# Kernel optimization log

Hardware: AMD Instinct MI355X
Metric: run time of the kernel (lower is better)

The kernel has to match this reference:

```python
import jax, jax.numpy as jnp
import numpy as np

B, L, W, C = 16, 200, 64, 128
H_INTRA = 64   # intra_hidden // 2 per direction
H_INTER = 128
EPS = 1e-8


def layer_norm(x, gamma, beta):
    mu = jnp.mean(x, axis=-1, keepdims=True)
    var = jnp.mean(jnp.square(x - mu), axis=-1, keepdims=True)
    return (x - mu) * jax.lax.rsqrt(var + EPS) * gamma + beta


def gru_seq(x, Wk, Uk, b, H):
    """Keras GRU, reset_after=False, recurrent_activation=sigmoid. x: [N,T,D] -> [N,T,H]."""
    xw = jnp.einsum('ntd,dk->ntk', x, Wk) + b  # precompute input projections [N,T,3H]
    def step(h, xw_t):
        z = jax.nn.sigmoid(xw_t[:, :H] + h @ Uk[:, :H])
        r = jax.nn.sigmoid(xw_t[:, H:2 * H] + h @ Uk[:, H:2 * H])
        hh = jnp.tanh(xw_t[:, 2 * H:] + (r * h) @ Uk[:, 2 * H:])
        h = z * h + (1.0 - z) * hh
        return h, h
    h0 = jnp.zeros((x.shape[0], H), x.dtype)
    _, ys = jax.lax.scan(step, h0, jnp.swapaxes(xw, 0, 1))  # [T,N,H]
    return jnp.swapaxes(ys, 0, 1)


def skip_gru_seq(x, Wk, Uk, b, Wp, bp, H):
    """Skip-RNN GRU (Campos et al.): binary update gate u_t conditionally updates state.
    Returns (outputs [N,T,H], gates [N,T,1])."""
    xw = jnp.einsum('ntd,dk->ntk', x, Wk) + b
    def step(carry, xw_t):
        h, ut = carry
        # straight-through binarization of cumulative update prob
        u = ut + jax.lax.stop_gradient(jnp.round(ut) - ut)  # [N,1]
        z = jax.nn.sigmoid(xw_t[:, :H] + h @ Uk[:, :H])
        r = jax.nn.sigmoid(xw_t[:, H:2 * H] + h @ Uk[:, H:2 * H])
        hh = jnp.tanh(xw_t[:, 2 * H:] + (r * h) @ Uk[:, 2 * H:])
        h_new = z * h + (1.0 - z) * hh
        h = u * h_new + (1.0 - u) * h  # skip: copy state when u == 0
        delta = jax.nn.sigmoid(h @ Wp + bp)  # [N,1]
        ut_next = u * delta + (1.0 - u) * (ut + jnp.minimum(delta, 1.0 - ut))
        return (h, ut_next), (h, u)
    N = x.shape[0]
    h0 = jnp.zeros((N, H), x.dtype)
    ut0 = jnp.ones((N, 1), x.dtype)
    _, (ys, us) = jax.lax.scan(step, (h0, ut0), jnp.swapaxes(xw, 0, 1))
    return jnp.swapaxes(ys, 0, 1), jnp.swapaxes(us, 0, 1)


def setup_inputs():
    key = jax.random.key(0)
    ks = jax.random.split(key, 16)
    rn = lambda k, s: jax.random.normal(k, s, dtype=jnp.float32) * 0.05
    z = lambda s: jnp.zeros(s, jnp.float32)
    o = lambda s: jnp.ones(s, jnp.float32)
    return {
        'x': jax.random.normal(ks[0], (B, L, W, C), dtype=jnp.float32),
        'scale': jax.random.uniform(ks[1], (B, L, W, 1), dtype=jnp.float32),
        'Wf': rn(ks[2], (C, 3 * H_INTRA)), 'Uf': rn(ks[3], (H_INTRA, 3 * H_INTRA)), 'bf': z((3 * H_INTRA,)),
        'Wb': rn(ks[4], (C, 3 * H_INTRA)), 'Ub': rn(ks[5], (H_INTRA, 3 * H_INTRA)), 'bb': z((3 * H_INTRA,)),
        'W_intra_fc': rn(ks[6], (2 * H_INTRA, C)), 'b_intra_fc': z((C,)),
        'g_intra': o((C,)), 'beta_intra': z((C,)),
        'Wi': rn(ks[7], (C + 1, 3 * H_INTER)), 'Ui': rn(ks[8], (H_INTER, 3 * H_INTER)), 'bi': z((3 * H_INTER,)),
        'Wp': rn(ks[9], (H_INTER, 1)), 'bp': z((1,)),
        'W_inter_fc': rn(ks[10], (H_INTER, C)), 'b_inter_fc': z((C,)),
        'g_inter': o((C,)), 'beta_inter': z((C,)),
    }


def reference(x, scale, Wf, Uf, bf, Wb, Ub, bb, W_intra_fc, b_intra_fc, g_intra, beta_intra,
              Wi, Ui, bi, Wp, bp, W_inter_fc, b_inter_fc, g_inter, beta_inter):
    # ----- intra path: bidirectional GRU over the width axis -----
    intra_in = x.reshape(B * L, W, C)
    out_f = gru_seq(intra_in, Wf, Uf, bf, H_INTRA)
    out_b = gru_seq(intra_in[:, ::-1, :], Wb, Ub, bb, H_INTRA)[:, ::-1, :]
    intra_rnn_out = jnp.concatenate([out_f, out_b], axis=-1)  # [B*L, W, 2H]
    update_gate_intra = jnp.ones((64, L), jnp.float32)  # skip=0 branch: constant ones
    intra_dense = intra_rnn_out @ W_intra_fc + b_intra_fc  # [B*L, W, C]
    intra_out = x + layer_norm(intra_dense.reshape(B, L, W, C), g_intra, beta_intra)
    # ----- inter path: skip-GRU over the L (time) axis -----
    inter_in = jnp.transpose(intra_out, (0, 2, 1, 3)).reshape(B * W, L, C)
    scale2 = jnp.transpose(scale, (0, 2, 1, 3)).reshape(B * W, L, 1)
    inter_in = jnp.concatenate([inter_in, scale2], axis=-1)  # [B*W, L, C+1]
    inter_rnn_out, gates = skip_gru_seq(inter_in, Wi, Ui, bi, Wp, bp, H_INTER)
    update_gate_inter = gates[:, :, 0]  # [B*W, L]
    inter_dense = (inter_rnn_out @ W_inter_fc + b_inter_fc).reshape(B, W, L, C)
    inter_ln_in = jnp.transpose(inter_dense, (0, 2, 1, 3))  # [B, L, W, C]
    inter_out = intra_out + layer_norm(inter_ln_in, g_inter, beta_inter)
    return inter_out, update_gate_intra, update_gate_inter
```

## Files before the change

### kernel.cpp

```cpp
#include <hip/hip_runtime.h>
#include <cmath>


__device__ __forceinline__ float sigf(float x) { return 1.0f / (1.0f + expf(-x)); }
__device__ __forceinline__ float rlanef(float v, int l) {
  return __uint_as_float(__builtin_amdgcn_readlane(__float_as_uint(v), (unsigned)l));
}

__global__ __launch_bounds__(256) void k_fill_ones(float* __restrict__ p, int n) {
  int i = blockIdx.x * 256 + threadIdx.x;
  if (i < n) p[i] = 1.0f;
}

enum { MA_X_FWD = 0, MA_X_BWD = 1, MA_INTER = 2 };

template <int MODE>
__global__ __launch_bounds__(256) void k_gemm_xw(
    const float* __restrict__ A0, const float* __restrict__ A1,
    const float* __restrict__ Bm, const float* __restrict__ bias,
    float* __restrict__ Cm, long M0, int N, int K, int KT)
{
  __shared__ float As[16][68];
  __shared__ float Bs[16][68];
  const int tid = threadIdx.x;
  const int tx = tid & 15, ty = tid >> 4;
  const long row0g = M0 + (long)blockIdx.x * 64;
  const int col0 = blockIdx.y * 64;
  const int lr = tid >> 2;
  const int lk4 = (tid & 3) * 4;
  const int bk = tid >> 4;
  const int bc4 = (tid & 15) * 4;
  float acc[4][4];
#pragma unroll
  for (int i = 0; i < 4; ++i)
#pragma unroll
    for (int j = 0; j < 4; ++j) acc[i][j] = 0.f;

  for (int kt = 0; kt < KT; ++kt) {
    const int k0 = kt * 16;
    {
      const long rg = row0g + lr;
      float v0, v1, v2, v3;
      if (MODE == MA_X_FWD) {
        const float4 a4 = *reinterpret_cast<const float4*>(&A0[rg * 128 + k0 + lk4]);
        v0 = a4.x; v1 = a4.y; v2 = a4.z; v3 = a4.w;
      } else if (MODE == MA_X_BWD) {
        const long s = rg >> 6; const int t = (int)(rg & 63);
        const float4 a4 =
            *reinterpret_cast<const float4*>(&A0[(s * 64 + (63 - t)) * 128 + k0 + lk4]);
        v0 = a4.x; v1 = a4.y; v2 = a4.z; v3 = a4.w;
      } else {
        const int n = (int)(rg & 1023);
        const int l = (int)(rg >> 10);
        const long rowc = ((long)(n >> 6) * 200 + l) * 64 + (n & 63);
        const long base = rowc * 128;
        if (kt < 8) {
          const float4 a4 = *reinterpret_cast<const float4*>(&A0[base + k0 + lk4]);
          v0 = a4.x; v1 = a4.y; v2 = a4.z; v3 = a4.w;
        } else {
          v0 = (lk4 == 0) ? A1[rowc] : 0.f;
          v1 = 0.f; v2 = 0.f; v3 = 0.f;
        }
      }
      As[lk4 + 0][lr] = v0;
      As[lk4 + 1][lr] = v1;
      As[lk4 + 2][lr] = v2;
      As[lk4 + 3][lr] = v3;
    }
    {
      const int k = k0 + bk;
      float4 b4 = make_float4(0.f, 0.f, 0.f, 0.f);
      if (k < K) b4 = *reinterpret_cast<const float4*>(&Bm[(long)k * N + col0 + bc4]);
      *reinterpret_cast<float4*>(&Bs[bk][bc4]) = b4;
    }
    __syncthreads();
#pragma unroll
    for (int kk = 0; kk < 16; ++kk) {
      const float4 a4 = *reinterpret_cast<const float4*>(&As[kk][ty * 4]);
      const float4 b4 = *reinterpret_cast<const float4*>(&Bs[kk][tx * 4]);
      const float av[4] = {a4.x, a4.y, a4.z, a4.w};
      const float bv[4] = {b4.x, b4.y, b4.z, b4.w};
#pragma unroll
      for (int i = 0; i < 4; ++i)
#pragma unroll
        for (int j = 0; j < 4; ++j) acc[i][j] = fmaf(av[i], bv[j], acc[i][j]);
    }
    __syncthreads();
  }
  const float4 bi4 = *reinterpret_cast<const float4*>(&bias[col0 + tx * 4]);
  const float bv[4] = {bi4.x, bi4.y, bi4.z, bi4.w};
#pragma unroll
  for (int i = 0; i < 4; ++i) {
    const long rl = (long)blockIdx.x * 64 + ty * 4 + i;
    float4 o;
    o.x = acc[i][0] + bv[0];
    o.y = acc[i][1] + bv[1];
    o.z = acc[i][2] + bv[2];
    o.w = acc[i][3] + bv[3];
    *reinterpret_cast<float4*>(&Cm[rl * (long)N + col0 + tx * 4]) = o;
  }
}

__global__ __launch_bounds__(256, 4) void k_gru_intra2(
    const float* __restrict__ xwf, const float* __restrict__ xwb,
    const float* __restrict__ Uf, const float* __restrict__ Ub,
    float* __restrict__ rnn)
{
  const int dir = blockIdx.y;
  const float* __restrict__ xw = dir ? xwb : xwf;
  const float* __restrict__ U  = dir ? Ub : Uf;
  __shared__ float h8[4][64], z8[4][64], rh8[4][64];
  __shared__ float pA[4][2][128];
  __shared__ float pB[4][2][64];
  const int tid = threadIdx.x;
  const int w = tid >> 6, lane = tid & 63;
  const long s0 = (long)blockIdx.x * 4;
  const bool isZR = (w < 2);
  const int ksZ = w;
  const int ksH = w - 2;

  float ua[32], ub[32];
  if (isZR) {
#pragma unroll
    for (int k = 0; k < 32; ++k) {
      ua[k] = U[(ksZ * 32 + k) * 192 + lane];
      ub[k] = U[(ksZ * 32 + k) * 192 + 64 + lane];
    }
  } else {
#pragma unroll
    for (int k = 0; k < 32; ++k)
      ua[k] = U[(ksH * 32 + k) * 192 + 128 + lane];
  }
  h8[w][lane] = 0.f;
  __syncthreads();

  const long xrow0 = (s0 + w) * 64;
  float xa1 = xw[xrow0 * 192 + lane];
  float xa2 = xw[xrow0 * 192 + 64 + lane];
  float xb  = xw[xrow0 * 192 + 128 + lane];

  for (int t = 0; t < 64; ++t) {
    const int tn = (t < 63) ? t + 1 : t;
    const float xa1n = xw[(xrow0 + tn) * 192 + lane];
    const float xa2n = xw[(xrow0 + tn) * 192 + 64 + lane];
    const float xbn  = xw[(xrow0 + tn) * 192 + 128 + lane];
    if (isZR) {
      const float hv0 = h8[lane >> 5][ksZ * 32 + (lane & 31)];
      const float hv1 = h8[2 + (lane >> 5)][ksZ * 32 + (lane & 31)];
      float az[4], ar[4];
#pragma unroll
      for (int s = 0; s < 4; ++s) { az[s] = 0.f; ar[s] = 0.f; }
#pragma unroll
      for (int s = 0; s < 4; ++s) {
        const float hvr = (s < 2) ? hv0 : hv1;
#pragma unroll
        for (int k = 0; k < 32; ++k) {
          const float hs = rlanef(hvr, ((s & 1) << 5) | k);
          az[s] = fmaf(ua[k], hs, az[s]);
          ar[s] = fmaf(ub[k], hs, ar[s]);
        }
      }
#pragma unroll
      for (int s = 0; s < 4; ++s) {
        pA[s][ksZ][lane] = az[s];
        pA[s][ksZ][64 + lane] = ar[s];
      }
    }
    __syncthreads();
    {
      const float sz = pA[w][0][lane] + pA[w][1][lane] + xa1;
      const float sr = pA[w][0][64 + lane] + pA[w][1][64 + lane] + xa2;
      z8[w][lane] = sigf(sz);
      rh8[w][lane] = sigf(sr) * h8[w][lane];
    }
    __syncthreads();
    if (!isZR) {
      const float rv0 = rh8[lane >> 5][ksH * 32 + (lane & 31)];
      const float rv1 = rh8[2 + (lane >> 5)][ksH * 32 + (lane & 31)];
      float ah[4];
#pragma unroll
      for (int s = 0; s < 4; ++s) ah[s] = 0.f;
#pragma unroll
      for (int s = 0; s < 4; ++s) {
        const float rvr = (s < 2) ? rv0 : rv1;
#pragma unroll
        for (int k = 0; k < 32; ++k) {
          const float rs = rlanef(rvr, ((s & 1) << 5) | k);
          ah[s] = fmaf(ua[k], rs, ah[s]);
        }
      }
#pragma unroll
      for (int s = 0; s < 4; ++s) pB[s][ksH][lane] = ah[s];
    }
    __syncthreads();
    {
      const float pre = pB[w][0][lane] + pB[w][1][lane] + xb;
      const float hh = tanhf(pre);
      const float z = z8[w][lane];
      const float ho = h8[w][lane];
      const float hn = z * ho + (1.f - z) * hh;
      h8[w][lane] = hn;
      const int tt = dir ? (63 - t) : t;
      rnn[((s0 + w) * 64 + tt) * 128 + dir * 64 + lane] = hn;
    }
    __syncthreads();
    xa1 = xa1n; xa2 = xa2n; xb = xbn;
  }
}

__global__ __launch_bounds__(1024, 4) void k_gru_inter3(
    const float* __restrict__ xw, const float* __restrict__ Ui,
    const float* __restrict__ Wp, const float* __restrict__ bp,
    float* __restrict__ rnn, float* __restrict__ gates,
    float* __restrict__ hstate, float* __restrict__ ustate,
    int t0, int nt)
{
  __shared__ float h4[4][128], z4[4][128], rh4[4][128];
  __shared__ float pA[4][8][256];
  __shared__ float pB[4][8][128];
  __shared__ float uu[4], utt[4];
  const int tid = threadIdx.x;
  const int w = tid >> 6, lane = tid & 63;
  const int n0 = blockIdx.x * 4;
  const bool isZR = (w < 8);

  float ureg[64];
  if (isZR) {
#pragma unroll
    for (int j = 0; j < 4; ++j)
#pragma unroll
      for (int k = 0; k < 16; ++k)
        ureg[j * 16 + k] = Ui[(long)(w * 16 + k) * 384 + j * 64 + lane];
  } else {
    const int ks = w - 8;
#pragma unroll
    for (int j = 0; j < 2; ++j)
#pragma unroll
      for (int k = 0; k < 16; ++k)
        ureg[j * 16 + k] = Ui[(long)(ks * 16 + k) * 384 + 256 + j * 64 + lane];
  }
  if (tid < 512) {
    const int s = tid >> 7, c = tid & 127;
    h4[s][c] = (t0 == 0) ? 0.f : hstate[(long)(n0 + s) * 128 + c];
  }
  if (tid < 4) {
    utt[tid] = (t0 == 0) ? 1.f : ustate[n0 + tid];
    uu[tid]  = (t0 == 0) ? 1.f : ustate[1024 + n0 + tid];
  }
  const float bp0 = bp[0];
  float wprA = 0.f, wprB = 0.f;
  if (w < 4) { wprA = Wp[lane]; wprB = Wp[64 + lane]; }
  __syncthreads();

  const int cs = w >> 2;
  const int cc = (w & 3) * 64 + lane;
  float xc = xw[(long)(n0 + cs) * 384 + cc];
  float xbA = 0.f, xbB = 0.f;
  if (w < 4) {
    xbA = xw[(long)(n0 + w) * 384 + 256 + lane];
    xbB = xw[(long)(n0 + w) * 384 + 320 + lane];
  }

  for (int dl = 0; dl < nt; ++dl) {
    const float u0g = uu[0], u1g = uu[1], u2g = uu[2], u3g = uu[3];
    const bool act = (u0g + u1g + u2g + u3g) != 0.f;
    const int dn = (dl + 1 < nt) ? dl + 1 : dl;
    const float xcn = xw[((long)dn * 1024 + n0 + cs) * 384 + cc];
    float xbAn = 0.f, xbBn = 0.f;
    if (w < 4) {
      xbAn = xw[((long)dn * 1024 + n0 + w) * 384 + 256 + lane];
      xbBn = xw[((long)dn * 1024 + n0 + w) * 384 + 320 + lane];
    }
    if (act) {
      if (isZR) {
        const float hv = h4[lane >> 4][w * 16 + (lane & 15)];
        float acc[4][4];
#pragma unroll
        for (int j = 0; j < 4; ++j)
#pragma unroll
          for (int s = 0; s < 4; ++s) acc[j][s] = 0.f;
#pragma unroll
        for (int s = 0; s < 4; ++s) {
          const float ug = (s == 0) ? u0g : (s == 1) ? u1g : (s == 2) ? u2g : u3g;
          if (ug != 0.f) {
#pragma unroll
            for (int k = 0; k < 16; ++k) {
              const float hs = rlanef(hv, (s << 4) | k);
              acc[0][s] = fmaf(ureg[k], hs, acc[0][s]);
              acc[1][s] = fmaf(ureg[16 + k], hs, acc[1][s]);
              acc[2][s] = fmaf(ureg[32 + k], hs, acc[2][s]);
              acc[3][s] = fmaf(ureg[48 + k], hs, acc[3][s]);
            }
#pragma unroll
            for (int j = 0; j < 4; ++j) pA[s][w][j * 64 + lane] = acc[j][s];
          }
        }
      }
      __syncthreads();
      {
        const float ugc = uu[cs];
        if (ugc != 0.f) {
          float sum = xc;
#pragma unroll
          for (int ks = 0; ks < 8; ++ks) sum += pA[cs][ks][cc];
          if (cc < 128) z4[cs][cc] = sigf(sum);
          else rh4[cs][cc - 128] = sigf(sum) * h4[cs][cc - 128];
        }
      }
      __syncthreads();
      if (!isZR) {
        const int ks = w - 8;
        const float rv = rh4[lane >> 4][ks * 16 + (lane & 15)];
        float acc0[4], acc1[4];
#pragma unroll
        for (int s = 0; s < 4; ++s) { acc0[s] = 0.f; acc1[s] = 0.f; }
#pragma unroll
        for (int s = 0; s < 4; ++s) {
          const float ug = (s == 0) ? u0g : (s == 1) ? u1g : (s == 2) ? u2g : u3g;
          if (ug != 0.f) {
#pragma unroll
            for (int k = 0; k < 16; ++k) {
              const float rs = rlanef(rv, (s << 4) | k);
              acc0[s] = fmaf(ureg[k], rs, acc0[s]);
              acc1[s] = fmaf(ureg[16 + k], rs, acc1[s]);
            }
            pB[s][ks][lane] = acc0[s];
            pB[s][ks][64 + lane] = acc1[s];
          }
        }
      }
      __syncthreads();
    }
    if (w < 4) {
      const float us = uu[w];
      const float hoA = h4[w][lane], hoB = h4[w][64 + lane];
      float hqA, hqB;
      if (us != 0.f) {
        float sA = xbA, sB = xbB;
#pragma unroll
        for (int ks = 0; ks < 8; ++ks) {
          sA += pB[w][ks][lane];
          sB += pB[w][ks][64 + lane];
        }
        const float hhA = tanhf(sA), hhB = tanhf(sB);
        const float zA = z4[w][lane], zB = z4[w][64 + lane];
        hqA = zA * hoA + (1.f - zA) * hhA;
        hqB = zB * hoB + (1.f - zB) * hhB;
        h4[w][lane] = hqA;
        h4[w][64 + lane] = hqB;
      } else {
        hqA = hoA; hqB = hoB;
      }
      rnn[((long)dl * 1024 + n0 + w) * 128 + lane] = hqA;
      rnn[((long)dl * 1024 + n0 + w) * 128 + 64 + lane] = hqB;
      float p = hqA * wprA + hqB * wprB;
      p += __shfl_xor(p, 32);
      p += __shfl_xor(p, 16);
      p += __shfl_xor(p, 8);
      p += __shfl_xor(p, 4);
      p += __shfl_xor(p, 2);
      p += __shfl_xor(p, 1);
      const float delta = sigf(p + bp0);
      const float ut = utt[w];
      const float utn = us * delta + (1.f - us) * (ut + fminf(delta, 1.f - ut));
      if (lane == 0) {
        gates[(long)(n0 + w) * 200 + t0 + dl] = us;
        utt[w] = utn;
        uu[w] = rintf(utn);
      }
    }
    __syncthreads();
    xc = xcn; xbA = xbAn; xbB = xbBn;
  }
  if (tid < 512) {
    const int s = tid >> 7, c = tid & 127;
    hstate[(long)(n0 + s) * 128 + c] = h4[s][c];
  }
  if (tid < 4) {
    ustate[n0 + tid] = utt[tid];
    ustate[1024 + n0 + tid] = uu[tid];
  }
}

template <int OM>
__global__ __launch_bounds__(256) void k_fcln(
    const float* __restrict__ A, const float* __restrict__ Wt,
    const float* __restrict__ bias, const float* __restrict__ gamma,
    const float* __restrict__ beta, const float* __restrict__ resid,
    float* __restrict__ dst, long M0)
{
  __shared__ float As[16][36];
  __shared__ float Bs[16][132];
  __shared__ float red0[32][33];
  __shared__ float red1[32][33];
  __shared__ float mu_s[32];
  __shared__ float rs_s[32];
  const int tid = threadIdx.x;
  const int tx = tid & 31, ty = tid >> 5;
  const long r0l = (long)blockIdx.x * 32;
  const int lr = tid >> 3;
  const int lk2 = (tid & 7) * 2;
  const int bkk = tid >> 4;
  const int bc8 = (tid & 15) * 8;
  float acc[4][4];
#pragma unroll
  for (int i = 0; i < 4; ++i)
#pragma unroll
    for (int j = 0; j < 4; ++j) acc[i][j] = 0.f;

  for (int kt = 0; kt < 8; ++kt) {
    const int k0 = kt * 16;
    const float2 a2 = *reinterpret_cast<const float2*>(&A[(r0l + lr) * 128 + k0 + lk2]);
    As[lk2][lr] = a2.x;
    As[lk2 + 1][lr] = a2.y;
    const float4 w0 = *reinterpret_cast<const float4*>(&Wt[(long)(k0 + bkk) * 128 + bc8]);
    const float4 w1 = *reinterpret_cast<const float4*>(&Wt[(long)(k0 + bkk) * 128 + bc8 + 4]);
    *reinterpret_cast<float4*>(&Bs[bkk][bc8]) = w0;
    *reinterpret_cast<float4*>(&Bs[bkk][bc8 + 4]) = w1;
    __syncthreads();
#pragma unroll
    for (int kk = 0; kk < 16; ++kk) {
      const float4 a4 = *reinterpret_cast<const float4*>(&As[kk][ty * 4]);
      const float4 b4 = *reinterpret_cast<const float4*>(&Bs[kk][tx * 4]);
      const float av[4] = {a4.x, a4.y, a4.z, a4.w};
      const float bv[4] = {b4.x, b4.y, b4.z, b4.w};
#pragma unroll
      for (int i = 0; i < 4; ++i)
#pragma unroll
        for (int j = 0; j < 4; ++j) acc[i][j] = fmaf(av[i], bv[j], acc[i][j]);
    }
    __syncthreads();
  }
  {
    const float4 bb4 = *reinterpret_cast<const float4*>(&bias[tx * 4]);
    const float bv[4] = {bb4.x, bb4.y, bb4.z, bb4.w};
#pragma unroll
    for (int i = 0; i < 4; ++i)
#pragma unroll
      for (int j = 0; j < 4; ++j) acc[i][j] += bv[j];
  }
#pragma unroll
  for (int i = 0; i < 4; ++i) {
    const float s = acc[i][0] + acc[i][1] + acc[i][2] + acc[i][3];
    const float q = acc[i][0] * acc[i][0] + acc[i][1] * acc[i][1] +
                    acc[i][2] * acc[i][2] + acc[i][3] * acc[i][3];
    red0[ty * 4 + i][tx] = s;
    red1[ty * 4 + i][tx] = q;
  }
  __syncthreads();
  if (tid < 32) {
    float s = 0.f, q = 0.f;
#pragma unroll
    for (int j = 0; j < 32; ++j) { s += red0[tid][j]; q += red1[tid][j]; }
    const float mu = s * (1.0f / 128.0f);
    const float var = q * (1.0f / 128.0f) - mu * mu;
    mu_s[tid] = mu;
    rs_s[tid] = 1.0f / sqrtf(var + 1e-8f);
  }
  __syncthreads();
  const float4 g4 = *reinterpret_cast<const float4*>(&gamma[tx * 4]);
  const float4 be4 = *reinterpret_cast<const float4*>(&beta[tx * 4]);
#pragma unroll
  for (int i = 0; i < 4; ++i) {
    const int rloc = ty * 4 + i;
    const long rg = M0 + r0l + rloc;
    long off;
    if (OM == 0) {
      off = rg * 128 + tx * 4;
    } else {
      const int n = (int)(rg & 1023);
      const int l = (int)(rg >> 10);
      off = (((long)(n >> 6) * 200 + l) * 64 + (n & 63)) * 128 + tx * 4;
    }
    const float4 r4 = *reinterpret_cast<const float4*>(&resid[off]);
    const float mu = mu_s[rloc], rs = rs_s[rloc];
    float4 o;
    o.x = (acc[i][0] - mu) * rs * g4.x + be4.x + r4.x;
    o.y = (acc[i][1] - mu) * rs * g4.y + be4.y + r4.y;
    o.z = (acc[i][2] - mu) * rs * g4.z + be4.z + r4.z;
    o.w = (acc[i][3] - mu) * rs * g4.w + be4.w + r4.w;
    *reinterpret_cast<float4*>(&dst[off]) = o;
  }
}

extern "C" void kernel_launch(void* const* d_in, const int* in_sizes, int n_in,
                              void* d_out, int out_size, void* d_ws, size_t ws_size,
                              hipStream_t stream)
{
  (void)in_sizes; (void)n_in; (void)out_size;
  const float* x    = (const float*)d_in[0];
  const float* scl  = (const float*)d_in[1];
  const float* Wf   = (const float*)d_in[2];
  const float* Uf   = (const float*)d_in[3];
  const float* bf   = (const float*)d_in[4];
  const float* Wb   = (const float*)d_in[5];
  const float* Ub   = (const float*)d_in[6];
  const float* bb   = (const float*)d_in[7];
  const float* Wfc1 = (const float*)d_in[8];
  const float* bfc1 = (const float*)d_in[9];
  const float* gam1 = (const float*)d_in[10];
  const float* bet1 = (const float*)d_in[11];
  const float* Wi   = (const float*)d_in[12];
  const float* Ui   = (const float*)d_in[13];
  const float* bi   = (const float*)d_in[14];
  const float* Wp   = (const float*)d_in[15];
  const float* bp   = (const float*)d_in[16];
  const float* Wfc2 = (const float*)d_in[17];
  const float* bfc2 = (const float*)d_in[18];
  const float* gam2 = (const float*)d_in[19];
  const float* bet2 = (const float*)d_in[20];

  float* outp  = (float*)d_out;
  float* io    = outp;
  float* onesp = outp + 26214400L;
  float* gates = outp + 26214400L + 12800L;
  float* ws    = (float*)d_ws;
  const long wsf = (long)(ws_size / sizeof(float));

  k_fill_ones<<<50, 256, 0, stream>>>(onesp, 12800);

  long cnI = (wsf / 32768L) & ~7L;
  if (cnI > 3200) cnI = 3200;
  if (cnI < 8) cnI = 8;
  for (long s0 = 0; s0 < 3200; s0 += cnI) {
    const long cn = (3200 - s0 < cnI) ? (3200 - s0) : cnI;
    float* xwf = ws;
    float* xwb = ws + cn * 12288L;
    float* rnn = ws + cn * 24576L;
    const long M = cn * 64;
    dim3 gg((unsigned)(M / 64), 3);
    k_gemm_xw<MA_X_FWD><<<gg, 256, 0, stream>>>(x, nullptr, Wf, bf, xwf, s0 * 64, 192, 128, 8);
    k_gemm_xw<MA_X_BWD><<<gg, 256, 0, stream>>>(x, nullptr, Wb, bb, xwb, s0 * 64, 192, 128, 8);
    dim3 gr((unsigned)(cn / 4), 2);
    k_gru_intra2<<<gr, 256, 0, stream>>>(xwf, xwb, Uf, Ub, rnn);
    k_fcln<0><<<(unsigned)(M / 32), 256, 0, stream>>>(rnn, Wfc1, bfc1, gam1, bet1, x, io, s0 * 64);
  }

  const long per_t = 1024L * 384 + 1024L * 128;
  const long state_f = 1024L * 128 + 3072L;
  long nt_alloc = (wsf - state_f) / per_t;
  if (nt_alloc > 200) nt_alloc = 200;
  if (nt_alloc < 1) nt_alloc = 1;
  float* xwi    = ws;
  float* rnnI   = ws + nt_alloc * 1024L * 384;
  float* hstate = rnnI + nt_alloc * 1024L * 128;
  float* ustate = hstate + 1024L * 128;

  for (long t0 = 0; t0 < 200; t0 += nt_alloc) {
    const int nt = (int)((200 - t0 < nt_alloc) ? (200 - t0) : nt_alloc);
    dim3 gg((unsigned)(16 * nt), 6);
    k_gemm_xw<MA_INTER><<<gg, 256, 0, stream>>>(io, scl, Wi, bi, xwi, t0 * 1024, 384, 129, 9);
    k_gru_inter3<<<256, 1024, 0, stream>>>(xwi, Ui, Wp, bp, rnnI, gates, hstate, ustate,
                                           (int)t0, nt);
    k_fcln<1><<<(unsigned)(32 * nt), 256, 0, stream>>>(rnnI, Wfc2, bfc2, gam2, bet2, io, outp,
                                                       t0 * 1024);
  }
}
```

Measured before the change: 1.884 ms.

## Split GRU recurrent matvecs across all waves instead of role-specialized waves

```diff
diff --git a/kernel.cpp b/kernel.cpp
--- a/kernel.cpp
+++ b/kernel.cpp
@@ -1,10 +1,28 @@
 #include <hip/hip_runtime.h>
 #include <cmath>
 
+
+typedef float f32x16 __attribute__((ext_vector_type(16)));
 
 __device__ __forceinline__ float sigf(float x) { return 1.0f / (1.0f + expf(-x)); }
 __device__ __forceinline__ float rlanef(float v, int l) {
   return __uint_as_float(__builtin_amdgcn_readlane(__float_as_uint(v), (unsigned)l));
+}
+
+template <int SB>
+__device__ __forceinline__ void macP2(const f32x16& u0, const f32x16& u1, float hv,
+                                      float& a0, float& a1) {
+#pragma unroll
+  for (int k = 0; k < 16; ++k) {
+    const float hs = rlanef(hv, SB + k);
+    a0 = fmaf(u0[k], hs, a0);
+    a1 = fmaf(u1[k], hs, a1);
+  }
+}
+template <int SB>
+__device__ __forceinline__ void macP1(const f32x16& u, float hv, float& a) {
+#pragma unroll
+  for (int k = 0; k < 16; ++k) a = fmaf(u[k], rlanef(hv, SB + k), a);
 }
 
 __global__ __launch_bounds__(256) void k_fill_ones(float* __restrict__ p, int n) {
@@ -101,7 +119,7 @@
   }
 }
 
-__global__ __launch_bounds__(256, 4) void k_gru_intra2(
+__global__ __launch_bounds__(256, 4) void k_gru_intra4(
     const float* __restrict__ xwf, const float* __restrict__ xwb,
     const float* __restrict__ Uf, const float* __restrict__ Ub,
     float* __restrict__ rnn)
@@ -110,26 +128,19 @@
   const float* __restrict__ xw = dir ? xwb : xwf;
   const float* __restrict__ U  = dir ? Ub : Uf;
   __shared__ float h8[4][64], z8[4][64], rh8[4][64];
-  __shared__ float pA[4][2][128];
-  __shared__ float pB[4][2][64];
+  __shared__ float pA[4][4][128];
+  __shared__ float pB[4][4][64];
   const int tid = threadIdx.x;
   const int w = tid >> 6, lane = tid & 63;
   const long s0 = (long)blockIdx.x * 4;
-  const bool isZR = (w < 2);
-  const int ksZ = w;
-  const int ksH = w - 2;
-
-  float ua[32], ub[32];
-  if (isZR) {
-#pragma unroll
-    for (int k = 0; k < 32; ++k) {
-      ua[k] = U[(ksZ * 32 + k) * 192 + lane];
-      ub[k] = U[(ksZ * 32 + k) * 192 + 64 + lane];
-    }
-  } else {
-#pragma unroll
-    for (int k = 0; k < 32; ++k)
-      ua[k] = U[(ksH * 32 + k) * 192 + 128 + lane];
+
+  f32x16 uz, ur, uhh;
+#pragma unroll
+  for (int k = 0; k < 16; ++k) {
+    const int row = (w * 16 + k) * 192;
+    uz[k]  = U[row + lane];
+    ur[k]  = U[row + 64 + lane];
+    uhh[k] = U[row + 128 + lane];
   }
   h8[w][lane] = 0.f;
   __syncthreads();
@@ -144,57 +155,47 @@
     const float xa1n = xw[(xrow0 + tn) * 192 + lane];
     const float xa2n = xw[(xrow0 + tn) * 192 + 64 + lane];
     const float xbn  = xw[(xrow0 + tn) * 192 + 128 + lane];
-    if (isZR) {
-      const float hv0 = h8[lane >> 5][ksZ * 32 + (lane & 31)];
-      const float hv1 = h8[2 + (lane >> 5)][ksZ * 32 + (lane & 31)];
-      float az[4], ar[4];
-#pragma unroll
-      for (int s = 0; s < 4; ++s) { az[s] = 0.f; ar[s] = 0.f; }
-#pragma unroll
-      for (int s = 0; s < 4; ++s) {
-        const float hvr = (s < 2) ? hv0 : hv1;
-#pragma unroll
-        for (int k = 0; k < 32; ++k) {
-          const float hs = rlanef(hvr, ((s & 1) << 5) | k);
-          az[s] = fmaf(ua[k], hs, az[s]);
-          ar[s] = fmaf(ub[k], hs, ar[s]);
-        }
-      }
-#pragma unroll
-      for (int s = 0; s < 4; ++s) {
-        pA[s][ksZ][lane] = az[s];
-        pA[s][ksZ][64 + lane] = ar[s];
-      }
-    }
-    __syncthreads();
     {
-      const float sz = pA[w][0][lane] + pA[w][1][lane] + xa1;
-      const float sr = pA[w][0][64 + lane] + pA[w][1][64 + lane] + xa2;
+      const float hv01 = h8[lane >> 5][w * 16 + (lane & 15)];
+      const float hv23 = h8[2 + (lane >> 5)][w * 16 + (lane & 15)];
+      float az0 = 0.f, ar0 = 0.f, az1 = 0.f, ar1 = 0.f;
+      float az2 = 0.f, ar2 = 0.f, az3 = 0.f, ar3 = 0.f;
+      macP2<0>(uz, ur, hv01, az0, ar0);
+      macP2<32>(uz, ur, hv01, az1, ar1);
+      macP2<0>(uz, ur, hv23, az2, ar2);
+      macP2<32>(uz, ur, hv23, az3, ar3);
+      pA[0][w][lane] = az0; pA[0][w][64 + lane] = ar0;
+      pA[1][w][lane] = az1; pA[1][w][64 + lane] = ar1;
+      pA[2][w][lane] = az2; pA[2][w][64 + lane] = ar2;
+      pA[3][w][lane] = az3; pA[3][w][64 + lane] = ar3;
+    }
+    __syncthreads();
+    {
+      const float sz = pA[w][0][lane] + pA[w][1][lane] + pA[w][2][lane] +
+                       pA[w][3][lane] + xa1;
+      const float sr = pA[w][0][64 + lane] + pA[w][1][64 + lane] +
+                       pA[w][2][64 + lane] + pA[w][3][64 + lane] + xa2;
       z8[w][lane] = sigf(sz);
       rh8[w][lane] = sigf(sr) * h8[w][lane];
     }
     __syncthreads();
-    if (!isZR) {
-      const float rv0 = rh8[lane >> 5][ksH * 32 + (lane & 31)];
-      const float rv1 = rh8[2 + (lane >> 5)][ksH * 32 + (lane & 31)];
-      float ah[4];
-#pragma unroll
-      for (int s = 0; s < 4; ++s) ah[s] = 0.f;
-#pragma unroll
-      for (int s = 0; s < 4; ++s) {
-        const float rvr = (s < 2) ? rv0 : rv1;
-#pragma unroll
-        for (int k = 0; k < 32; ++k) {
-          const float rs = rlanef(rvr, ((s & 1) << 5) | k);
-          ah[s] = fmaf(ua[k], rs, ah[s]);
-        }
-      }
-#pragma unroll
-      for (int s = 0; s < 4; ++s) pB[s][ksH][lane] = ah[s];
-    }
-    __syncthreads();
     {
-      const float pre = pB[w][0][lane] + pB[w][1][lane] + xb;
+      const float rv01 = rh8[lane >> 5][w * 16 + (lane & 15)];
+      const float rv23 = rh8[2 + (lane >> 5)][w * 16 + (lane & 15)];
+      float a0 = 0.f, a1 = 0.f, a2 = 0.f, a3 = 0.f;
+      macP1<0>(uhh, rv01, a0);
+      macP1<32>(uhh, rv01, a1);
+      macP1<0>(uhh, rv23, a2);
+      macP1<32>(uhh, rv23, a3);
+      pB[0][w][lane] = a0;
+      pB[1][w][lane] = a1;
+      pB[2][w][lane] = a2;
+      pB[3][w][lane] = a3;
+    }
+    __syncthreads();
+    {
+      const float pre = pB[w][0][lane] + pB[w][1][lane] + pB[w][2][lane] +
+                        pB[w][3][lane] + xb;
       const float hh = tanhf(pre);
       const float z = z8[w][lane];
       const float ho = h8[w][lane];
@@ -208,7 +209,7 @@
   }
 }
 
-__global__ __launch_bounds__(1024, 4) void k_gru_inter3(
+__global__ __launch_bounds__(1024, 4) void k_gru_inter5(
     const float* __restrict__ xw, const float* __restrict__ Ui,
     const float* __restrict__ Wp, const float* __restrict__ bp,
     float* __restrict__ rnn, float* __restrict__ gates,
@@ -222,22 +223,16 @@
   const int tid = threadIdx.x;
   const int w = tid >> 6, lane = tid & 63;
   const int n0 = blockIdx.x * 4;
-  const bool isZR = (w < 8);
-
-  float ureg[64];
-  if (isZR) {
-#pragma unroll
-    for (int j = 0; j < 4; ++j)
-#pragma unroll
-      for (int k = 0; k < 16; ++k)
-        ureg[j * 16 + k] = Ui[(long)(w * 16 + k) * 384 + j * 64 + lane];
-  } else {
-    const int ks = w - 8;
-#pragma unroll
-    for (int j = 0; j < 2; ++j)
-#pragma unroll
-      for (int k = 0; k < 16; ++k)
-        ureg[j * 16 + k] = Ui[(long)(ks * 16 + k) * 384 + 256 + j * 64 + lane];
+  const int kA = (w & 7) * 16;
+  const int cH = w >> 3;
+
+  f32x16 uzA, uzB, uh;
+#pragma unroll
+  for (int k = 0; k < 16; ++k) {
+    const long r = (long)(kA + k) * 384;
+    uzA[k] = Ui[r + cH * 128 + lane];
+    uzB[k] = Ui[r + cH * 128 + 64 + lane];
+    uh[k]  = Ui[r + 256 + cH * 64 + lane];
   }
   if (tid < 512) {
     const int s = tid >> 7, c = tid & 127;
@@ -252,9 +247,9 @@
   if (w < 4) { wprA = Wp[lane]; wprB = Wp[64 + lane]; }
   __syncthreads();
 
-  const int cs = w >> 2;
-  const int cc = (w & 3) * 64 + lane;
-  float xc = xw[(long)(n0 + cs) * 384 + cc];
+  const int sC = tid >> 8;
+  const int cC = tid & 255;
+  float xc = xw[(long)(n0 + sC) * 384 + cC];
   float xbA = 0.f, xbB = 0.f;
   if (w < 4) {
     xbA = xw[(long)(n0 + w) * 384 + 256 + lane];
@@ -265,68 +260,72 @@
     const float u0g = uu[0], u1g = uu[1], u2g = uu[2], u3g = uu[3];
     const bool act = (u0g + u1g + u2g + u3g) != 0.f;
     const int dn = (dl + 1 < nt) ? dl + 1 : dl;
-    const float xcn = xw[((long)dn * 1024 + n0 + cs) * 384 + cc];
+    const float xcn = xw[((long)dn * 1024 + n0 + sC) * 384 + cC];
     float xbAn = 0.f, xbBn = 0.f;
     if (w < 4) {
       xbAn = xw[((long)dn * 1024 + n0 + w) * 384 + 256 + lane];
       xbBn = xw[((long)dn * 1024 + n0 + w) * 384 + 320 + lane];
     }
     if (act) {
-      if (isZR) {
-        const float hv = h4[lane >> 4][w * 16 + (lane & 15)];
-        float acc[4][4];
-#pragma unroll
-        for (int j = 0; j < 4; ++j)
-#pragma unroll
-          for (int s = 0; s < 4; ++s) acc[j][s] = 0.f;
-#pragma unroll
-        for (int s = 0; s < 4; ++s) {
-          const float ug = (s == 0) ? u0g : (s == 1) ? u1g : (s == 2) ? u2g : u3g;
-          if (ug != 0.f) {
-#pragma unroll
-            for (int k = 0; k < 16; ++k) {
-              const float hs = rlanef(hv, (s << 4) | k);
-              acc[0][s] = fmaf(ureg[k], hs, acc[0][s]);
-              acc[1][s] = fmaf(ureg[16 + k], hs, acc[1][s]);
-              acc[2][s] = fmaf(ureg[32 + k], hs, acc[2][s]);
-              acc[3][s] = fmaf(ureg[48 + k], hs, acc[3][s]);
-            }
-#pragma unroll
-            for (int j = 0; j < 4; ++j) pA[s][w][j * 64 + lane] = acc[j][s];
-          }
+      {
+        const float hv01 = h4[lane >> 5][kA + (lane & 15)];
+        const float hv23 = h4[2 + (lane >> 5)][kA + (lane & 15)];
+        const int kq = w & 7;
+        if (u0g != 0.f) {
+          float a0 = 0.f, a1 = 0.f;
+          macP2<0>(uzA, uzB, hv01, a0, a1);
+          pA[0][kq][cH * 128 + lane] = a0;
+          pA[0][kq][cH * 128 + 64 + lane] = a1;
+        }
+        if (u1g != 0.f) {
+          float a0 = 0.f, a1 = 0.f;
+          macP2<32>(uzA, uzB, hv01, a0, a1);
+          pA[1][kq][cH * 128 + lane] = a0;
+          pA[1][kq][cH * 128 + 64 + lane] = a1;
+        }
+        if (u2g != 0.f) {
+          float a0 = 0.f, a1 = 0.f;
+          macP2<0>(uzA, uzB, hv23, a0, a1);
+          pA[2][kq][cH * 128 + lane] = a0;
+          pA[2][kq][cH * 128 + 64 + lane] = a1;
+        }
+        if (u3g != 0.f) {
+          float a0 = 0.f, a1 = 0.f;
+          macP2<32>(uzA, uzB, hv23, a0, a1);
+          pA[3][kq][cH * 128 + lane] = a0;
+          pA[3][kq][cH * 128 + 64 + lane] = a1;
         }
       }
       __syncthreads();
       {
-        const float ugc = uu[cs];
-        if (ugc != 0.f) {
+        if (uu[sC] != 0.f) {
           float sum = xc;
 #pragma unroll
-          for (int ks = 0; ks < 8; ++ks) sum += pA[cs][ks][cc];
-          if (cc < 128) z4[cs][cc] = sigf(sum);
-          else rh4[cs][cc - 128] = sigf(sum) * h4[cs][cc - 128];
+          for (int q = 0; q < 8; ++q) sum += pA[sC][q][cC];
+          if (cC < 128) z4[sC][cC] = sigf(sum);
+          else rh4[sC][cC - 128] = sigf(sum) * h4[sC][cC - 128];
         }
       }
       __syncthreads();
-      if (!isZR) {
-        const int ks = w - 8;
-        const float rv = rh4[lane >> 4][ks * 16 + (lane & 15)];
-        float acc0[4], acc1[4];
-#pragma unroll
-        for (int s = 0; s < 4; ++s) { acc0[s] = 0.f; acc1[s] = 0.f; }
-#pragma unroll
-        for (int s = 0; s < 4; ++s) {
-          const float ug = (s == 0) ? u0g : (s == 1) ? u1g : (s == 2) ? u2g : u3g;
-          if (ug != 0.f) {
-#pragma unroll
-            for (int k = 0; k < 16; ++k) {
-              const float rs = rlanef(rv, (s << 4) | k);
-              acc0[s] = fmaf(ureg[k], rs, acc0[s]);
-              acc1[s] = fmaf(ureg[16 + k], rs, acc1[s]);
-            }
-            pB[s][ks][lane] = acc0[s];
-            pB[s][ks][64 + lane] = acc1[s];
-          }
+      {
+        const float rv01 = rh4[lane >> 5][kA + (lane & 15)];
+        const float rv23 = rh4[2 + (lane >> 5)][kA + (lane & 15)];
+        const int kq = w & 7;
+        if (u0g != 0.f) {
+          float b = 0.f; macP1<0>(uh, rv01, b);
+          pB[0][kq][cH * 64 + lane] = b;
+        }
+        if (u1g != 0.f) {
+          float b = 0.f; macP1<32>(uh, rv01, b);
+          pB[1][kq][cH * 64 + lane] = b;
+        }
+        if (u2g != 0.f) {
+          float b = 0.f; macP1<0>(uh, rv23, b);
+          pB[2][kq][cH * 64 + lane] = b;
+        }
+        if (u3g != 0.f) {
+          float b = 0.f; macP1<32>(uh, rv23, b);
+          pB[3][kq][cH * 64 + lane] = b;
         }
       }
       __syncthreads();
@@ -338,9 +337,9 @@
       if (us != 0.f) {
         float sA = xbA, sB = xbB;
 #pragma unroll
-        for (int ks = 0; ks < 8; ++ks) {
-          sA += pB[w][ks][lane];
-          sB += pB[w][ks][64 + lane];
+        for (int q = 0; q < 8; ++q) {
+          sA += pB[w][q][lane];
+          sB += pB[w][q][64 + lane];
         }
         const float hhA = tanhf(sA), hhB = tanhf(sB);
         const float zA = z4[w][lane], zB = z4[w][64 + lane];
@@ -532,7 +531,7 @@
     k_gemm_xw<MA_X_FWD><<<gg, 256, 0, stream>>>(x, nullptr, Wf, bf, xwf, s0 * 64, 192, 128, 8);
     k_gemm_xw<MA_X_BWD><<<gg, 256, 0, stream>>>(x, nullptr, Wb, bb, xwb, s0 * 64, 192, 128, 8);
     dim3 gr((unsigned)(cn / 4), 2);
-    k_gru_intra2<<<gr, 256, 0, stream>>>(xwf, xwb, Uf, Ub, rnn);
+    k_gru_intra4<<<gr, 256, 0, stream>>>(xwf, xwb, Uf, Ub, rnn);
     k_fcln<0><<<(unsigned)(M / 32), 256, 0, stream>>>(rnn, Wfc1, bfc1, gam1, bet1, x, io, s0 * 64);
   }
 
@@ -550,7 +549,7 @@
     const int nt = (int)((200 - t0 < nt_alloc) ? (200 - t0) : nt_alloc);
     dim3 gg((unsigned)(16 * nt), 6);
     k_gemm_xw<MA_INTER><<<gg, 256, 0, stream>>>(io, scl, Wi, bi, xwi, t0 * 1024, 384, 129, 9);
-    k_gru_inter3<<<256, 1024, 0, stream>>>(xwi, Ui, Wp, bp, rnnI, gates, hstate, ustate,
+    k_gru_inter5<<<256, 1024, 0, stream>>>(xwi, Ui, Wp, bp, rnnI, gates, hstate, ustate,
                                            (int)t0, nt);
     k_fcln<1><<<(unsigned)(32 * nt), 256, 0, stream>>>(rnnI, Wfc2, bfc2, gam2, bet2, io, outp,
                                                        t0 * 1024);
```

New measurement: 1.792 ms. -4.9%, faster.
